# Optimization experiments

Hardware: AMD Instinct MI355X
Metric: run time of the kernel (lower is better)

Reference implementation:

```python
import jax, jax.numpy as jnp
import numpy as np

D_MODEL = 1024
D_INNER = 2048   # expand=2
D_STATE = 16
D_CONV = 4
DT_RANK = 64     # ceil(d_model/16)
BATCH = 4
SEQLEN = 2048


def setup_inputs() -> dict:
    key = jax.random.key(0)
    ks = jax.random.split(key, 9)
    f = lambda k, shape, s=0.02: jax.random.normal(k, shape, dtype=jnp.float32) * s
    return {
        "x": jax.random.normal(ks[0], (BATCH, SEQLEN, D_MODEL), dtype=jnp.float32),
        "norm_w": jnp.ones((D_MODEL,), jnp.float32),
        "in_proj_w": f(ks[1], (2 * D_INNER, D_MODEL)),
        "conv_w": f(ks[2], (D_INNER, D_CONV), 0.1),
        "conv_b": f(ks[3], (D_INNER,), 0.1),
        "x_proj_w": f(ks[4], (DT_RANK + 2 * D_STATE, D_INNER)),
        "dt_proj_w": f(ks[5], (D_INNER, DT_RANK), 0.1),
        "dt_proj_b": f(ks[6], (D_INNER,), 0.1),
        "A_log": jnp.log(jnp.tile(jnp.arange(1, D_STATE + 1, dtype=jnp.float32), (D_INNER, 1))),
        "D_param": jnp.ones((D_INNER,), jnp.float32),
        "out_proj_w": f(ks[7], (D_MODEL, D_INNER)),
    }


def _rmsnorm(x, w):
    eps = jnp.finfo(jnp.float32).eps
    var = jnp.mean(x * x, axis=-1, keepdims=True)
    return x * jax.lax.rsqrt(var + eps) * w


def _mamba(x_norm, in_proj_w, conv_w, conv_b, x_proj_w,
           dt_proj_w, dt_proj_b, A_log, D_param, out_proj_w):
    B, L, _ = x_norm.shape
    # input projection -> [B, L, 2*D_INNER], split into x and gate z
    xz = jnp.einsum('bld,ed->ble', x_norm, in_proj_w)
    x_in, z = jnp.split(xz, 2, axis=-1)
    # causal depthwise conv1d (kernel D_CONV, left pad D_CONV-1)
    x_c = jax.lax.conv_general_dilated(
        x_in.transpose(0, 2, 1),                 # [B, D_INNER, L]
        conv_w[:, None, :],                      # [D_INNER, 1, D_CONV]
        window_strides=(1,), padding=[(D_CONV - 1, 0)],
        dimension_numbers=('NCH', 'OIH', 'NCH'),
        feature_group_count=D_INNER,
    ) + conv_b[None, :, None]
    u = jax.nn.silu(x_c.transpose(0, 2, 1))      # [B, L, D_INNER]
    # SSM parameters
    x_dbl = jnp.einsum('bld,ed->ble', u, x_proj_w)  # [B, L, DT_RANK+2*D_STATE]
    dt, B_mat, C_mat = jnp.split(x_dbl, [DT_RANK, DT_RANK + D_STATE], axis=-1)
    dt = jax.nn.softplus(jnp.einsum('blr,dr->bld', dt, dt_proj_w) + dt_proj_b)  # [B,L,D_INNER]
    A = -jnp.exp(A_log)                          # [D_INNER, D_STATE]

    # selective scan over time; state h: [B, D_INNER, D_STATE]
    def step(h, inputs):
        dt_t, B_t, C_t, u_t = inputs             # [B,Dn],[B,S],[B,S],[B,Dn]
        dA = jnp.exp(dt_t[:, :, None] * A)       # [B, Dn, S]
        h = dA * h + (dt_t * u_t)[:, :, None] * B_t[:, None, :]
        y_t = jnp.einsum('bds,bs->bd', h, C_t)
        return h, y_t

    h0 = jnp.zeros((B, D_INNER, D_STATE), x_norm.dtype)
    xs = (dt.transpose(1, 0, 2), B_mat.transpose(1, 0, 2),
          C_mat.transpose(1, 0, 2), u.transpose(1, 0, 2))
    _, ys = jax.lax.scan(step, h0, xs)           # [L, B, D_INNER]
    y = ys.transpose(1, 0, 2) + D_param * u
    y = y * jax.nn.silu(z)
    return jnp.einsum('bld,ed->ble', y, out_proj_w)  # [B, L, D_MODEL]


def reference(x, norm_w, in_proj_w, conv_w, conv_b, x_proj_w,
              dt_proj_w, dt_proj_b, A_log, D_param, out_proj_w):
    x_norm = _rmsnorm(x, norm_w)
    out = _mamba(x_norm, in_proj_w, conv_w, conv_b, x_proj_w,
                 dt_proj_w, dt_proj_b, A_log, D_param, out_proj_w)
    return x + out
```

## Files before the change

kernel.cpp:

```cpp
#include <hip/hip_runtime.h>
#include <hip/hip_bf16.h>
#include <math.h>

#define DM 1024
#define DI 2048
#define DS 16
#define DC 4
#define DR 64
#define NB 4
#define SL 2048
#define BL (NB * SL)
#define DXP (DR + 2 * DS)
#define NC 32
#define CL (SL / NC)
#define XNS 8

typedef __hip_bfloat16 bf16;
typedef __attribute__((ext_vector_type(8))) short short8;
typedef __attribute__((ext_vector_type(4))) float floatx4;
typedef unsigned int u32;

__device__ __forceinline__ float to_f(float v) { return v; }
__device__ __forceinline__ float to_f(bf16 v) { return __bfloat162float(v); }
template <typename T> __device__ __forceinline__ T from_f(float v);
template <> __device__ __forceinline__ float from_f<float>(float v) { return v; }
template <> __device__ __forceinline__ bf16 from_f<bf16>(float v) { return __float2bfloat16(v); }

__device__ __forceinline__ float bfbits2f(unsigned short u) {
  u32 b = ((u32)u) << 16;
  return __builtin_bit_cast(float, b);
}
__device__ __forceinline__ ushort f2bfbits(float v) {
  bf16 b = __float2bfloat16(v);
  return (ushort)__builtin_bit_cast(short, b);
}
__device__ __forceinline__ float fsilu(float v) {
  return v * __builtin_amdgcn_rcpf(1.f + __expf(-v));
}

__device__ __forceinline__ void gload16(const ushort* g, ushort* l) {
  __builtin_amdgcn_global_load_lds((const __attribute__((address_space(1))) void*)g,
                                   (__attribute__((address_space(3))) void*)l,
                                   16, 0, 0);
}

__device__ __forceinline__ void vmw6() { asm volatile("s_waitcnt vmcnt(6)" ::: "memory"); }
__device__ __forceinline__ void vmw4() { asm volatile("s_waitcnt vmcnt(4)" ::: "memory"); }
__device__ __forceinline__ void vmw2() { asm volatile("s_waitcnt vmcnt(2)" ::: "memory"); }
__device__ __forceinline__ void vmw0() { asm volatile("s_waitcnt vmcnt(0)" ::: "memory"); }
__device__ __forceinline__ void barx() {
  asm volatile("" ::: "memory");
  __builtin_amdgcn_s_barrier();
  asm volatile("" ::: "memory");
}

__global__ __launch_bounds__(256) void f2b_k(const float* __restrict__ src,
                                             bf16* __restrict__ dst, int n) {
  int i = blockIdx.x * 256 + threadIdx.x;
  if (i < n) dst[i] = from_f<bf16>(src[i]);
}

__global__ __launch_bounds__(256) void rmsnorm_k(const float* __restrict__ x,
                                                 const float* __restrict__ w,
                                                 bf16* __restrict__ o) {
  int row = blockIdx.x;
  const float4* xr = (const float4*)(x + (size_t)row * DM);
  float4 v = xr[threadIdx.x];
  float ss = v.x * v.x + v.y * v.y + v.z * v.z + v.w * v.w;
  for (int off = 32; off > 0; off >>= 1) ss += __shfl_down(ss, off);
  __shared__ float sred[4];
  __shared__ float sscale;
  if ((threadIdx.x & 63) == 0) sred[threadIdx.x >> 6] = ss;
  __syncthreads();
  if (threadIdx.x == 0) {
    float t = sred[0] + sred[1] + sred[2] + sred[3];
    sscale = rsqrtf(t / (float)DM + 1.1920929e-7f);
  }
  __syncthreads();
  float sc = sscale;
  float4 wv = ((const float4*)w)[threadIdx.x];
  ushort4 pk;
  pk.x = f2bfbits(v.x * sc * wv.x);
  pk.y = f2bfbits(v.y * sc * wv.y);
  pk.z = f2bfbits(v.z * sc * wv.z);
  pk.w = f2bfbits(v.w * sc * wv.w);
  ((ushort4*)((ushort*)o + (size_t)row * DM))[threadIdx.x] = pk;
}

template <int MODE>
__global__ __launch_bounds__(512, 1) void gemm256(const bf16* __restrict__ A,
                                                  const bf16* __restrict__ W,
                                                  int M, int N, int K,
                                                  bf16* __restrict__ Cx,
                                                  bf16* __restrict__ Cz, int nsplit,
                                                  float* __restrict__ Cf,
                                                  const float* __restrict__ R) {
  __shared__ ushort SH[65536];
  const int tid = threadIdx.x;
  const int lane = tid & 63, wv = tid >> 6;
  const int wr = wv >> 2, wc = wv & 3;
  const int row15 = lane & 15, quad = lane >> 4;

  int ntm = M >> 8, ntn = N >> 8, nwg = ntm * ntn;
  int bid = blockIdx.x;
  int swz = (bid & 7) * (nwg >> 3) + (bid >> 3);
  int bm0 = (swz / ntn) << 8, bn0 = (swz % ntn) << 8;

  const int nt = K >> 6;
  const ushort* Au = (const ushort*)A;
  const ushort* Wu = (const ushort*)W;

  const int w4u = lane ^ (((lane >> 5) & 1) << 1);
  const int Wsw = (((row15 << 6) | (quad << 4)) ^ (((row15 >> 3) & 1) << 5));
  const char* SHb = (const char*)SH;
  const int Abase0 = (wr << 14) + Wsw;
  const int Abase1 = 32768 + (wr << 14) + Wsw;
  const int Bbase0 = 65536 + ((wc >> 1) << 14) + ((wc & 1) << 13) + Wsw;
  const int Bbase1 = Bbase0 + 32768;

  auto stageA = [&](int tt, int half, int buf) {
    const ushort* g = Au + (size_t)(bm0 + half * 128) * K + tt * 64;
    char* lds = (char*)SH + (size_t)(buf * 2 + half) * 16384;
#pragma unroll
    for (int i = 0; i < 2; ++i) {
      int sub = wv + i * 8;
      int r = ((sub >> 1) << 4) | (w4u >> 2);
      int ce = ((sub & 1) << 5) | ((w4u & 3) << 3);
      gload16(g + (size_t)r * K + ce, (ushort*)(lds + sub * 1024));
    }
  };
  auto stageB = [&](int tt, int half, int buf) {
    const ushort* g = Wu + (size_t)(bn0 + half * 128) * K + tt * 64;
    char* lds = (char*)SH + 65536 + (size_t)(buf * 2 + half) * 16384;
#pragma unroll
    for (int i = 0; i < 2; ++i) {
      int sub = wv + i * 8;
      int r = ((sub >> 1) << 4) | (w4u >> 2);
      int ce = ((sub & 1) << 5) | ((w4u & 3) << 3);
      gload16(g + (size_t)r * K + ce, (ushort*)(lds + sub * 1024));
    }
  };

  short8 a_f[4][2], bq[2][2][2];
  floatx4 acc[8][4] = {};

#define LDA_(base, mh) do { _Pragma("unroll") for (int mi = 0; mi < 4; ++mi) \
  { _Pragma("unroll") for (int kk = 0; kk < 2; ++kk) \
    a_f[mi][kk] = *(const short8*)(SHb + (base) + ((((mh)*4 + mi)*2 + kk) << 10)); } } while (0)
#define LDB_(base, nh) do { _Pragma("unroll") for (int ni = 0; ni < 2; ++ni) \
  { _Pragma("unroll") for (int kk = 0; kk < 2; ++kk) \
    bq[nh][ni][kk] = *(const short8*)(SHb + (base) + (((((nh)*2 + ni)*2 + kk)) << 10)); } } while (0)
#define MM_(mh, nh) do { __builtin_amdgcn_s_setprio(1); \
  _Pragma("unroll") for (int mi = 0; mi < 4; ++mi) \
  { _Pragma("unroll") for (int ni = 0; ni < 2; ++ni) \
    { _Pragma("unroll") for (int kk = 0; kk < 2; ++kk) \
      acc[(mh)*4+mi][(nh)*2+ni] = __builtin_amdgcn_mfma_f32_16x16x32_bf16( \
          bq[nh][ni][kk], a_f[mi][kk], acc[(mh)*4+mi][(nh)*2+ni], 0, 0, 0); } } \
  __builtin_amdgcn_s_setprio(0); } while (0)

#define TILE_(t, AB, BB, BBn, curbuf, nxtbuf) do { \
  int tp1 = (t) + 1, tp2 = (t) + 2; \
   \
  LDA_(AB, 0); \
  if (tp1 < nt) stageA(tp1, 0, nxtbuf); \
  barx(); MM_(0, 0); barx(); \
   \
  LDB_(BB, 1); \
  if (tp1 < nt) stageA(tp1, 1, nxtbuf); \
  barx(); MM_(0, 1); barx(); \
   \
  LDA_(AB, 1); \
  if (tp2 < nt) stageB(tp2, 0, curbuf); \
  barx(); MM_(1, 0); \
  if (tp1 < nt) { if (tp2 < nt) vmw6(); else vmw4(); } \
  barx(); \
   \
  if (tp1 < nt) LDB_(BBn, 0); \
  if (tp2 < nt) stageB(tp2, 1, curbuf); \
  barx(); MM_(1, 1); \
  if (tp2 < nt) vmw4(); else vmw0(); \
  barx(); \
} while (0)

  stageB(0, 0, 0); stageB(0, 1, 0); stageA(0, 0, 0); stageA(0, 1, 0);
  stageB(1, 0, 1); stageB(1, 1, 1);
  vmw4();
  barx();
  LDB_(Bbase0, 0);

  for (int t = 0; t < nt; t += 2) {
    TILE_(t,     Abase0, Bbase0, Bbase1, 0, 1);
    TILE_(t + 1, Abase1, Bbase1, Bbase0, 1, 0);
  }
#undef TILE_
#undef MM_
#undef LDB_
#undef LDA_

#pragma unroll
  for (int mi8 = 0; mi8 < 8; ++mi8) {
    int grow = bm0 + wr * 128 + mi8 * 16 + row15;
#pragma unroll
    for (int ni4 = 0; ni4 < 4; ++ni4) {
      int gc = bn0 + wc * 64 + ni4 * 16 + quad * 4;
      floatx4 v = acc[mi8][ni4];
      if (MODE == 1) {
        if (gc < nsplit) {
          ushort4 pk = {f2bfbits(v[0]), f2bfbits(v[1]), f2bfbits(v[2]), f2bfbits(v[3])};
          *(ushort4*)((ushort*)Cx + (size_t)grow * DI + gc) = pk;
        } else {
          ushort4 pk = {f2bfbits(fsilu(v[0])), f2bfbits(fsilu(v[1])),
                        f2bfbits(fsilu(v[2])), f2bfbits(fsilu(v[3]))};
          *(ushort4*)((ushort*)Cz + (size_t)grow * DI + (gc - nsplit)) = pk;
        }
      } else {
        size_t o = (size_t)grow * N + gc;
        float4 r4 = *(const float4*)&R[o];
        float4 o4 = {v[0] + r4.x, v[1] + r4.y, v[2] + r4.z, v[3] + r4.w};
        *(float4*)&Cf[o] = o4;
      }
    }
  }
}

template <int MODE>
__global__ __launch_bounds__(512, 1) void gemm_np(const bf16* __restrict__ A,
                                                  const bf16* __restrict__ W,
                                                  int M, int N, int K,
                                                  bf16* __restrict__ Cx,
                                                  bf16* __restrict__ Cz, int nsplit,
                                                  float* __restrict__ Cf,
                                                  const float* __restrict__ R) {
  __shared__ ushort SH[49152];
  const int tid = threadIdx.x;
  const int lane = tid & 63, wv = tid >> 6;
  const int wr = wv >> 1, wc = wv & 1;
  const int row15 = lane & 15, quad = lane >> 4;

  int ntm = M >> 8, ntn = N >> 7, nwg = ntm * ntn;
  int bid = blockIdx.x;
  int swz = (bid & 7) * (nwg >> 3) + (bid >> 3);
  int bm0 = (swz / ntn) << 8, bn0 = (swz % ntn) << 7;

  const int nt = K >> 6;
  const ushort* Au = (const ushort*)A;
  const ushort* Wu = (const ushort*)W;
  const ushort* Ag = Au + (u32)bm0 * (u32)K;
  const ushort* Bg = Wu + (u32)bn0 * (u32)K;

  const int w4u = lane ^ (((lane >> 5) & 1) << 1);
  const int sub0 = wv, sub1 = wv + 8;
  const int r0 = ((sub0 >> 1) << 4) | (w4u >> 2);
  const int c0 = ((sub0 & 1) << 5) | ((w4u & 3) << 3);
  const int r1 = ((sub1 >> 1) << 4) | (w4u >> 2);
  const int c1 = ((sub1 & 1) << 5) | ((w4u & 3) << 3);
  ushort* shA = (ushort*)SH;
  ushort* shB = (ushort*)SH + 32768;

  auto stage = [&](const ushort* gbase, int rowoff, int tt, ushort* lbase) {
    gload16(gbase + (u32)(rowoff + r0) * (u32)K + (u32)(tt * 64 + c0), lbase + (sub0 << 9));
    gload16(gbase + (u32)(rowoff + r1) * (u32)K + (u32)(tt * 64 + c1), lbase + (sub1 << 9));
  };

  const int Wsw = (((row15 << 6) | (quad << 4)) ^ (((row15 >> 3) & 1) << 5));
  const char* SHb = (const char*)SH;
  const int AB0 = (wr << 13) + Wsw;
  const int AB1 = 32768 + AB0;
  const int BB0 = 65536 + (wc << 13) + Wsw;
  const int BB1 = BB0 + 16384;

  short8 a0[2][2], a1[2][2], bq0A[2][2], bq0B[2][2], bq1[2][2];
  floatx4 acc[4][4] = {};

#define LDA_(dst, base, mh) do { _Pragma("unroll") for (int i_ = 0; i_ < 2; ++i_) \
  { _Pragma("unroll") for (int kk = 0; kk < 2; ++kk) \
    dst[i_][kk] = *(const short8*)(SHb + (base) + ((((mh)*2 + i_)*2 + kk) << 10)); } } while (0)
#define LDB_(dst, base, nh) do { _Pragma("unroll") for (int j_ = 0; j_ < 2; ++j_) \
  { _Pragma("unroll") for (int kk = 0; kk < 2; ++kk) \
    dst[j_][kk] = *(const short8*)(SHb + (base) + ((((nh)*2 + j_)*2 + kk) << 10)); } } while (0)
#define MM_(aset, bset, mh, nh) do { __builtin_amdgcn_s_setprio(1); \
  _Pragma("unroll") for (int i_ = 0; i_ < 2; ++i_) \
  { _Pragma("unroll") for (int j_ = 0; j_ < 2; ++j_) \
    { _Pragma("unroll") for (int kk = 0; kk < 2; ++kk) \
      acc[(mh)*2+i_][(nh)*2+j_] = __builtin_amdgcn_mfma_f32_16x16x32_bf16( \
          bset[j_][kk], aset[i_][kk], acc[(mh)*2+i_][(nh)*2+j_], 0, 0, 0); } } \
  __builtin_amdgcn_s_setprio(0); } while (0)

#define TILE_(t, ABc, BBc, ABn, BBn, BQU, BQF, CURB, NXTB) do { \
  int tp1 = (t) + 1, tp2 = (t) + 2; \
   \
  LDB_(bq1, BBc, 1); \
  if (tp1 < nt) stage(Ag, 0, tp1, shA + (NXTB) * 16384); \
  barx(); MM_(a0, BQU, 0, 0); barx(); \
   \
  LDA_(a1, ABc, 1); \
  if (tp1 < nt) stage(Ag, 128, tp1, shA + (NXTB) * 16384 + 8192); \
  barx(); MM_(a0, bq1, 0, 1); barx(); \
   \
  if (tp2 < nt) stage(Bg, 0, tp2, shB + (CURB) * 8192); \
  barx(); MM_(a1, bq1, 1, 1); \
  if (tp2 < nt) vmw2(); else vmw0(); \
  barx(); \
   \
  if (tp1 < nt) { LDA_(a0, ABn, 0); LDB_(BQF, BBn, 0); } \
  barx(); MM_(a1, BQU, 1, 0); barx(); \
} while (0)

  stage(Bg, 0, 0, shB);
  stage(Ag, 0, 0, shA);
  stage(Ag, 128, 0, shA + 8192);
  if (nt > 1) { stage(Bg, 0, 1, shB + 8192); vmw2(); } else { vmw0(); }
  barx();
  LDA_(a0, AB0, 0);
  LDB_(bq0A, BB0, 0);

  for (int t = 0; t < nt; t += 2) {
    TILE_(t,     AB0, BB0, AB1, BB1, bq0A, bq0B, 0, 1);
    TILE_(t + 1, AB1, BB1, AB0, BB0, bq0B, bq0A, 1, 0);
  }
#undef TILE_
#undef MM_
#undef LDB_
#undef LDA_

#pragma unroll
  for (int mi = 0; mi < 4; ++mi) {
    int grow = bm0 + wr * 64 + mi * 16 + row15;
#pragma unroll
    for (int ni = 0; ni < 4; ++ni) {
      int gc = bn0 + wc * 64 + ni * 16 + quad * 4;
      floatx4 v = acc[mi][ni];
      if (MODE == 1) {
        if (gc < nsplit) {
          ushort4 pk = {f2bfbits(v[0]), f2bfbits(v[1]), f2bfbits(v[2]), f2bfbits(v[3])};
          *(ushort4*)((ushort*)Cx + (size_t)grow * DI + gc) = pk;
        } else {
          ushort4 pk = {f2bfbits(fsilu(v[0])), f2bfbits(fsilu(v[1])),
                        f2bfbits(fsilu(v[2])), f2bfbits(fsilu(v[3]))};
          *(ushort4*)((ushort*)Cz + (size_t)grow * DI + (gc - nsplit)) = pk;
        }
      } else {
        size_t o = (size_t)grow * N + gc;
        float4 r4 = *(const float4*)&R[o];
        float4 o4 = {v[0] + r4.x, v[1] + r4.y, v[2] + r4.z, v[3] + r4.w};
        *(float4*)&Cf[o] = o4;
      }
    }
  }
}

#define TM 128
#define TN 128
#define TK 32
#define LDK 40
template <int MODE>
__global__ __launch_bounds__(256) void gemm_mfma(const bf16* __restrict__ A,
                                                 const bf16* __restrict__ W,
                                                 int M, int N, int K,
                                                 bf16* __restrict__ Cx,
                                                 bf16* __restrict__ Cz, int nsplit,
                                                 float* __restrict__ Cf,
                                                 const float* __restrict__ R,
                                                 const float* __restrict__ bias) {
  __shared__ ushort Asm[TM][TK];
  __shared__ ushort Bsm[TN][TK];
  int bm = blockIdx.y * TM, bn = blockIdx.x * TN;
  int tid = threadIdx.x;
  int lane = tid & 63, wave = tid >> 6;
  int wm = (wave & 1) * 64, wn = (wave >> 1) * 64;
  int row15 = lane & 15, quad = lane >> 4;

  int srow = lane >> 2;
  int scol = (lane & 3) * 8;
  int s0 = wave * 2, s1 = wave * 2 + 1;

  const ushort* Au = (const ushort*)A;
  const ushort* Wu = (const ushort*)W;
  const ushort* ag0 = Au + (size_t)(bm + s0 * 16 + srow) * K + scol;
  const ushort* ag1 = Au + (size_t)(bm + s1 * 16 + srow) * K + scol;
  const ushort* bg0 = Wu + (size_t)(bn + s0 * 16 + srow) * K + scol;
  const ushort* bg1 = Wu + (size_t)(bn + s1 * 16 + srow) * K + scol;
  ushort* la0 = &Asm[s0 * 16][0];
  ushort* la1 = &Asm[s1 * 16][0];
  ushort* lb0 = &Bsm[s0 * 16][0];
  ushort* lb1 = &Bsm[s1 * 16][0];

  floatx4 acc[4][4] = {};

  for (int k0 = 0; k0 < K; k0 += TK) {
    gload16(ag0 + k0, la0);
    gload16(ag1 + k0, la1);
    gload16(bg0 + k0, lb0);
    gload16(bg1 + k0, lb1);
    __syncthreads();
    short8 a_f[4], b_f[4];
#pragma unroll
    for (int i = 0; i < 4; ++i)
      a_f[i] = *(const short8*)&Asm[wm + i * 16 + row15][quad * 8];
#pragma unroll
    for (int j = 0; j < 4; ++j)
      b_f[j] = *(const short8*)&Bsm[wn + j * 16 + row15][quad * 8];
#pragma unroll
    for (int i = 0; i < 4; ++i)
#pragma unroll
      for (int j = 0; j < 4; ++j)
        acc[i][j] = __builtin_amdgcn_mfma_f32_16x16x32_bf16(b_f[j], a_f[i], acc[i][j], 0, 0, 0);
    __syncthreads();
  }
#pragma unroll
  for (int mi = 0; mi < 4; ++mi) {
    int grow = bm + wm + mi * 16 + row15;
#pragma unroll
    for (int ni = 0; ni < 4; ++ni) {
      int gc = bn + wn + ni * 16 + quad * 4;
      floatx4 v = acc[mi][ni];
      if (MODE == 1) {
        if (gc < nsplit) {
          ushort4 pk = {f2bfbits(v[0]), f2bfbits(v[1]), f2bfbits(v[2]), f2bfbits(v[3])};
          *(ushort4*)((ushort*)Cx + (size_t)grow * DI + gc) = pk;
        } else {
          ushort4 pk = {f2bfbits(fsilu(v[0])), f2bfbits(fsilu(v[1])),
                        f2bfbits(fsilu(v[2])), f2bfbits(fsilu(v[3]))};
          *(ushort4*)((ushort*)Cz + (size_t)grow * DI + (gc - nsplit)) = pk;
        }
      } else if (MODE == 2) {
        size_t o = (size_t)grow * N + gc;
        float4 r4 = *(const float4*)&R[o];
        float4 o4 = {v[0] + r4.x, v[1] + r4.y, v[2] + r4.z, v[3] + r4.w};
        *(float4*)&Cf[o] = o4;
      } else {
        float4 b4 = *(const float4*)&bias[gc];
        float t0 = v[0] + b4.x, t1 = v[1] + b4.y, t2 = v[2] + b4.z, t3 = v[3] + b4.w;
        float s0_ = (t0 > 20.f) ? t0 : __logf(1.f + __expf(t0));
        float s1_ = (t1 > 20.f) ? t1 : __logf(1.f + __expf(t1));
        float s2_ = (t2 > 20.f) ? t2 : __logf(1.f + __expf(t2));
        float s3_ = (t3 > 20.f) ? t3 : __logf(1.f + __expf(t3));
        ushort4 pk = {f2bfbits(s0_), f2bfbits(s1_), f2bfbits(s2_), f2bfbits(s3_)};
        *(ushort4*)((ushort*)Cx + (size_t)grow * N + gc) = pk;
      }
    }
  }
}

__global__ __launch_bounds__(256) void xproj_k(const bf16* __restrict__ u,
                                               const bf16* __restrict__ w,
                                               float* __restrict__ Ppart) {
  __shared__ ushort Asm[128][LDK];
  __shared__ ushort Bsm[96][LDK];
  int kbase = blockIdx.x * (DI / XNS);
  int bm = blockIdx.y * 128;
  int tid = threadIdx.x;
  int lane = tid & 63, wave = tid >> 6;
  int row15 = lane & 15, quad = lane >> 4;
  int srow = tid >> 1, skoff = (tid & 1) * 16;

  floatx4 acc[2][6] = {};
  const ushort* Au = (const ushort*)u;
  const ushort* Wu = (const ushort*)w;
  for (int k0 = kbase; k0 < kbase + (DI / XNS); k0 += TK) {
    const ushort* ag = Au + (size_t)(bm + srow) * DI + k0 + skoff;
    *(short8*)&Asm[srow][skoff]     = *(const short8*)ag;
    *(short8*)&Asm[srow][skoff + 8] = *(const short8*)(ag + 8);
    if (tid < 192) {
      const ushort* wg = Wu + (size_t)srow * DI + k0 + skoff;
      *(short8*)&Bsm[srow][skoff]     = *(const short8*)wg;
      *(short8*)&Bsm[srow][skoff + 8] = *(const short8*)(wg + 8);
    }
    __syncthreads();
    short8 a_f[2], b_f[6];
#pragma unroll
    for (int i = 0; i < 2; ++i)
      a_f[i] = *(const short8*)&Asm[wave * 32 + i * 16 + row15][quad * 8];
#pragma unroll
    for (int j = 0; j < 6; ++j)
      b_f[j] = *(const short8*)&Bsm[j * 16 + row15][quad * 8];
#pragma unroll
    for (int i = 0; i < 2; ++i)
#pragma unroll
      for (int j = 0; j < 6; ++j)
        acc[i][j] = __builtin_amdgcn_mfma_f32_16x16x32_bf16(b_f[j], a_f[i], acc[i][j], 0, 0, 0);
    __syncthreads();
  }
  float* P = Ppart + (size_t)blockIdx.x * ((size_t)BL * DXP);
#pragma unroll
  for (int mi = 0; mi < 2; ++mi) {
    int grow = bm + wave * 32 + mi * 16 + row15;
#pragma unroll
    for (int nj = 0; nj < 6; ++nj) {
      int gc = nj * 16 + quad * 4;
      floatx4 v = acc[mi][nj];
      float4 o4 = {v[0], v[1], v[2], v[3]};
      *(float4*)&P[(size_t)grow * DXP + gc] = o4;
    }
  }
}

__global__ __launch_bounds__(256) void xred_k(const float* __restrict__ Ppart,
                                              float* __restrict__ xdbl,
                                              bf16* __restrict__ dtin) {
  int i = blockIdx.x * 256 + threadIdx.x;
  float s = 0.f;
#pragma unroll
  for (int p = 0; p < XNS; ++p) s += Ppart[(size_t)p * ((size_t)BL * DXP) + i];
  xdbl[i] = s;
  int r = i / DXP, c = i - r * DXP;
  if (c < DR) dtin[r * DR + c] = from_f<bf16>(s);
}

#define TSTRIP 8
__global__ __launch_bounds__(256) void conv_silu_k(const bf16* __restrict__ xin,
                                                   const float* __restrict__ cw,
                                                   const float* __restrict__ cb,
                                                   bf16* __restrict__ u) {
  int blk = blockIdx.x;
  int b = blk >> 8;
  int l0 = (blk & 255) * TSTRIP;
  int c0 = threadIdx.x * 8;

  float4 cw4[8];
  const float4* cwp = (const float4*)cw;
#pragma unroll
  for (int j = 0; j < 8; ++j) cw4[j] = cwp[c0 + j];
  float cbv[8];
  {
    float4 cb0 = *(const float4*)&cb[c0];
    float4 cb1 = *(const float4*)&cb[c0 + 4];
    cbv[0] = cb0.x; cbv[1] = cb0.y; cbv[2] = cb0.z; cbv[3] = cb0.w;
    cbv[4] = cb1.x; cbv[5] = cb1.y; cbv[6] = cb1.z; cbv[7] = cb1.w;
  }

  const ushort* base = (const ushort*)xin + ((size_t)(b * SL + l0) * DI + c0);
  ushort* ubase = (ushort*)u + ((size_t)(b * SL + l0) * DI + c0);

  short8 zz = {};
  short8 w0 = zz, w1 = zz, w2 = zz;
  if (l0 >= 3) {
    w0 = *(const short8*)(base - 3 * DI);
    w1 = *(const short8*)(base - 2 * DI);
    w2 = *(const short8*)(base - 1 * DI);
  }
#pragma unroll
  for (int l = 0; l < TSTRIP; ++l) {
    short8 w3 = *(const short8*)(base + (ptrdiff_t)l * DI);
    short8 outv;
#pragma unroll
    for (int j = 0; j < 8; ++j) {
      float a = cbv[j]
              + bfbits2f((unsigned short)w0[j]) * cw4[j].x
              + bfbits2f((unsigned short)w1[j]) * cw4[j].y
              + bfbits2f((unsigned short)w2[j]) * cw4[j].z
              + bfbits2f((unsigned short)w3[j]) * cw4[j].w;
      outv[j] = (short)f2bfbits(fsilu(a));
    }
    *(short8*)(ubase + (ptrdiff_t)l * DI) = outv;
    w0 = w1; w1 = w2; w2 = w3;
  }
}

__global__ __launch_bounds__(256) void scan_p1(const bf16* __restrict__ dts,
                                               const bf16* __restrict__ u,
                                               const float* __restrict__ xdbl,
                                               const float* __restrict__ A_log,
                                               float* __restrict__ Pbuf,
                                               float* __restrict__ Qbuf) {
  int bid = blockIdx.x;
  int b = bid >> 8;
  int c = (bid >> 3) & (NC - 1);
  int d = (bid & 7) * 256 + threadIdx.x;

  float A[DS], h[DS], P[DS];
#pragma unroll
  for (int s = 0; s < DS; ++s) {
    A[s] = -__expf(A_log[d * DS + s]);
    h[s] = 0.f; P[s] = 1.f;
  }
  size_t bl0 = (size_t)b * SL + c * CL;
  size_t base = bl0 * DI + d;
  size_t xb = bl0 * DXP + DR;
  for (int l = 0; l < CL; ++l) {
    float dtv = to_f(dts[base]);
    float uv = to_f(u[base]);
    float du = dtv * uv;
    float Bv[16];
    *(float4*)&Bv[0]  = *(const float4*)(xdbl + xb);
    *(float4*)&Bv[4]  = *(const float4*)(xdbl + xb + 4);
    *(float4*)&Bv[8]  = *(const float4*)(xdbl + xb + 8);
    *(float4*)&Bv[12] = *(const float4*)(xdbl + xb + 12);
#pragma unroll
    for (int s = 0; s < DS; ++s) {
      float dA = __expf(dtv * A[s]);
      h[s] = dA * h[s] + du * Bv[s];
      P[s] *= dA;
    }
    base += DI;
    xb += DXP;
  }
  size_t o = ((size_t)(b * NC + c) * DS) * DI + d;
#pragma unroll
  for (int s = 0; s < DS; ++s) {
    Pbuf[o + (size_t)s * DI] = P[s];
    Qbuf[o + (size_t)s * DI] = h[s];
  }
}

__global__ __launch_bounds__(256) void scan_p2(float* __restrict__ Pbuf,
                                               float* __restrict__ Qbuf) {
  int bid = blockIdx.x;
  int b = bid >> 7;
  int s = (bid >> 3) & (DS - 1);
  int d = (bid & 7) * 256 + threadIdx.x;
  float h = 0.f;
  for (int c = 0; c < NC; ++c) {
    size_t idx = ((size_t)((b * NC + c) * DS + s)) * DI + d;
    float Pv = Pbuf[idx];
    float qv = Qbuf[idx];
    Qbuf[idx] = h;
    h = Pv * h + qv;
  }
}

__global__ __launch_bounds__(256) void scan_p3(const bf16* __restrict__ dts,
                                               bf16* __restrict__ u,
                                               const float* __restrict__ xdbl,
                                               const float* __restrict__ A_log,
                                               const float* __restrict__ Dp,
                                               const bf16* __restrict__ g,
                                               const float* __restrict__ Qbuf) {
  int bid = blockIdx.x;
  int b = bid >> 8;
  int c = (bid >> 3) & (NC - 1);
  int d = (bid & 7) * 256 + threadIdx.x;

  float A[DS], h[DS];
  size_t o = ((size_t)(b * NC + c) * DS) * DI + d;
#pragma unroll
  for (int s = 0; s < DS; ++s) {
    A[s] = -__expf(A_log[d * DS + s]);
    h[s] = Qbuf[o + (size_t)s * DI];
  }
  float Dd = Dp[d];
  size_t bl0 = (size_t)b * SL + c * CL;
  size_t base = bl0 * DI + d;
  size_t xb = bl0 * DXP + DR;
  for (int l = 0; l < CL; ++l) {
    float dtv = to_f(dts[base]);
    float uv = to_f(u[base]);
    float gv = to_f(g[base]);
    float du = dtv * uv;
    float Bv[16], Cv[16];
    *(float4*)&Bv[0]  = *(const float4*)(xdbl + xb);
    *(float4*)&Bv[4]  = *(const float4*)(xdbl + xb + 4);
    *(float4*)&Bv[8]  = *(const float4*)(xdbl + xb + 8);
    *(float4*)&Bv[12] = *(const float4*)(xdbl + xb + 12);
    *(float4*)&Cv[0]  = *(const float4*)(xdbl + xb + DS);
    *(float4*)&Cv[4]  = *(const float4*)(xdbl + xb + DS + 4);
    *(float4*)&Cv[8]  = *(const float4*)(xdbl + xb + DS + 8);
    *(float4*)&Cv[12] = *(const float4*)(xdbl + xb + DS + 12);
    float p0 = 0.f, p1 = 0.f, p2 = 0.f, p3 = 0.f;
#pragma unroll
    for (int s = 0; s < DS; s += 4) {
      float dA0 = __expf(dtv * A[s + 0]);
      float dA1 = __expf(dtv * A[s + 1]);
      float dA2 = __expf(dtv * A[s + 2]);
      float dA3 = __expf(dtv * A[s + 3]);
      h[s + 0] = dA0 * h[s + 0] + du * Bv[s + 0];
      h[s + 1] = dA1 * h[s + 1] + du * Bv[s + 1];
      h[s + 2] = dA2 * h[s + 2] + du * Bv[s + 2];
      h[s + 3] = dA3 * h[s + 3] + du * Bv[s + 3];
      p0 += h[s + 0] * Cv[s + 0];
      p1 += h[s + 1] * Cv[s + 1];
      p2 += h[s + 2] * Cv[s + 2];
      p3 += h[s + 3] * Cv[s + 3];
    }
    float yv = ((p0 + p1) + (p2 + p3)) + Dd * uv;
    u[base] = from_f<bf16>(yv * gv);
    base += DI;
    xb += DXP;
  }
}

extern "C" void kernel_launch(void* const* d_in, const int* in_sizes, int n_in,
                              void* d_out, int out_size, void* d_ws, size_t ws_size,
                              hipStream_t stream) {
  const float* x        = (const float*)d_in[0];
  const float* norm_w   = (const float*)d_in[1];
  const float* in_projw = (const float*)d_in[2];
  const float* conv_w   = (const float*)d_in[3];
  const float* conv_b   = (const float*)d_in[4];
  const float* x_projw  = (const float*)d_in[5];
  const float* dt_projw = (const float*)d_in[6];
  const float* dt_projb = (const float*)d_in[7];
  const float* A_log    = (const float*)d_in[8];
  const float* Dp       = (const float*)d_in[9];
  const float* out_projw= (const float*)d_in[10];
  float* out = (float*)d_out;

  char* wsb = (char*)d_ws;
  bf16* x_buf  = (bf16*)wsb;
  bf16* z_buf  = (bf16*)(wsb + (size_t)BL * DI * 2);
  bf16* u_buf  = (bf16*)(wsb + (size_t)BL * DI * 4);
  char* ovl    = wsb + (size_t)BL * DI * 6;
  bf16* ipw_bf = (bf16*)ovl;
  float* xdbl   = (float*)ovl;
  bf16*  xpw_bf = (bf16*)(ovl + 3145728);
  bf16*  dtw_bf = (bf16*)(ovl + 3538944);
  bf16*  dtin_bf= (bf16*)(ovl + 3801088);
  bf16* xnorm_bf = u_buf;
  bf16* dt_buf   = x_buf;
  bf16* opw_bf   = x_buf;
  float* Ppart = out;
  float* Pbuf = out;
  float* Qbuf = out + (size_t)NB * NC * DS * DI;

  f2b_k<<<(2 * DI * DM) / 256, 256, 0, stream>>>(in_projw, ipw_bf, 2 * DI * DM);
  rmsnorm_k<<<BL, 256, 0, stream>>>(x, norm_w, xnorm_bf);
  gemm256<1><<<(BL / 256) * (2 * DI / 256), 512, 0, stream>>>(
      xnorm_bf, ipw_bf, BL, 2 * DI, DM, x_buf, z_buf, DI, nullptr, nullptr);
  conv_silu_k<<<NB * (SL / TSTRIP), 256, 0, stream>>>(x_buf, conv_w, conv_b, u_buf);
  f2b_k<<<(DXP * DI + 255) / 256, 256, 0, stream>>>(x_projw, xpw_bf, DXP * DI);
  f2b_k<<<(DI * DR) / 256, 256, 0, stream>>>(dt_projw, dtw_bf, DI * DR);
  xproj_k<<<dim3(XNS, BL / 128), 256, 0, stream>>>(u_buf, xpw_bf, Ppart);
  xred_k<<<(BL * DXP) / 256, 256, 0, stream>>>(Ppart, xdbl, dtin_bf);
  gemm_mfma<3><<<dim3(DI / TN, BL / TM), 256, 0, stream>>>(
      dtin_bf, dtw_bf, BL, DI, DR, dt_buf, nullptr, 0, nullptr, nullptr, dt_projb);
  scan_p1<<<NB * NC * (DI / 256), 256, 0, stream>>>(dt_buf, u_buf, xdbl, A_log, Pbuf, Qbuf);
  scan_p2<<<NB * DS * (DI / 256), 256, 0, stream>>>(Pbuf, Qbuf);
  scan_p3<<<NB * NC * (DI / 256), 256, 0, stream>>>(dt_buf, u_buf, xdbl, A_log, Dp, z_buf, Qbuf);
  f2b_k<<<(DM * DI) / 256, 256, 0, stream>>>(out_projw, opw_bf, DM * DI);
  gemm_np<2><<<(BL / 256) * (DM / 128), 512, 0, stream>>>(
      u_buf, opw_bf, BL, DM, DI, nullptr, nullptr, 0, out, x);
}
```

Measured before the change: 431.6 us.

## Prefetch A tiles two steps ahead in both bf16 GEMM pipelines

Both MFMA GEMM kernels change their global-to-LDS prefetch schedule so that A tiles are staged two iterations ahead into the current buffer, as B tiles already were. This deepens the pipeline: more loads are in flight and the vmcnt waits are relaxed accordingly. It also drops the early B-fragment register preload for the next tile in the large kernel. The aim is to hide more global-load latency behind MFMA work. In exchange, the LDS buffer reuse becomes more delicate, and more outstanding loads may add issue pressure.

```diff
diff --git a/kernel.cpp b/kernel.cpp
--- a/kernel.cpp
+++ b/kernel.cpp
@@ -46,7 +46,6 @@
 
 __device__ __forceinline__ void vmw6() { asm volatile("s_waitcnt vmcnt(6)" ::: "memory"); }
 __device__ __forceinline__ void vmw4() { asm volatile("s_waitcnt vmcnt(4)" ::: "memory"); }
-__device__ __forceinline__ void vmw2() { asm volatile("s_waitcnt vmcnt(2)" ::: "memory"); }
 __device__ __forceinline__ void vmw0() { asm volatile("s_waitcnt vmcnt(0)" ::: "memory"); }
 __device__ __forceinline__ void barx() {
   asm volatile("" ::: "memory");
@@ -158,39 +157,34 @@
           bq[nh][ni][kk], a_f[mi][kk], acc[(mh)*4+mi][(nh)*2+ni], 0, 0, 0); } } \
   __builtin_amdgcn_s_setprio(0); } while (0)
 
-#define TILE_(t, AB, BB, BBn, curbuf, nxtbuf) do { \
+#define TILE_(t, AB, BB, curbuf, nxtbuf) do { \
   int tp1 = (t) + 1, tp2 = (t) + 2; \
    \
-  LDA_(AB, 0); \
-  if (tp1 < nt) stageA(tp1, 0, nxtbuf); \
+  LDA_(AB, 0); LDB_(BB, 0); \
+  if (tp1 < nt) stageA(tp1, 1, nxtbuf); \
   barx(); MM_(0, 0); barx(); \
    \
   LDB_(BB, 1); \
-  if (tp1 < nt) stageA(tp1, 1, nxtbuf); \
   barx(); MM_(0, 1); barx(); \
    \
   LDA_(AB, 1); \
   if (tp2 < nt) stageB(tp2, 0, curbuf); \
-  barx(); MM_(1, 0); \
-  if (tp1 < nt) { if (tp2 < nt) vmw6(); else vmw4(); } \
-  barx(); \
+  barx(); MM_(1, 0); barx(); \
    \
-  if (tp1 < nt) LDB_(BBn, 0); \
-  if (tp2 < nt) stageB(tp2, 1, curbuf); \
+  if (tp2 < nt) { stageA(tp2, 0, curbuf); stageB(tp2, 1, curbuf); } \
   barx(); MM_(1, 1); \
-  if (tp2 < nt) vmw4(); else vmw0(); \
+  if (tp2 < nt) vmw6(); else vmw0(); \
   barx(); \
 } while (0)
 
   stageB(0, 0, 0); stageB(0, 1, 0); stageA(0, 0, 0); stageA(0, 1, 0);
-  stageB(1, 0, 1); stageB(1, 1, 1);
-  vmw4();
+  if (nt > 1) { stageB(1, 0, 1); stageB(1, 1, 1); stageA(1, 0, 1); vmw6(); }
+  else vmw0();
   barx();
-  LDB_(Bbase0, 0);
 
   for (int t = 0; t < nt; t += 2) {
-    TILE_(t,     Abase0, Bbase0, Bbase1, 0, 1);
-    TILE_(t + 1, Abase1, Bbase1, Bbase0, 1, 0);
+    TILE_(t, Abase0, Bbase0, 0, 1);
+    TILE_(t + 1, Abase1, Bbase1, 1, 0);
   }
 #undef TILE_
 #undef MM_
@@ -286,37 +280,42 @@
           bset[j_][kk], aset[i_][kk], acc[(mh)*2+i_][(nh)*2+j_], 0, 0, 0); } } \
   __builtin_amdgcn_s_setprio(0); } while (0)
 
-#define TILE_(t, ABc, BBc, ABn, BBn, BQU, BQF, CURB, NXTB) do { \
+#define TILE_(t, ABc, BBc, ABn, BBn, BQU, BQF, CURB) do { \
   int tp1 = (t) + 1, tp2 = (t) + 2; \
    \
   LDB_(bq1, BBc, 1); \
-  if (tp1 < nt) stage(Ag, 0, tp1, shA + (NXTB) * 16384); \
   barx(); MM_(a0, BQU, 0, 0); barx(); \
    \
   LDA_(a1, ABc, 1); \
-  if (tp1 < nt) stage(Ag, 128, tp1, shA + (NXTB) * 16384 + 8192); \
+  if (tp2 < nt) stage(Bg, 0, tp2, shB + (CURB) * 8192); \
   barx(); MM_(a0, bq1, 0, 1); barx(); \
    \
-  if (tp2 < nt) stage(Bg, 0, tp2, shB + (CURB) * 8192); \
+  if (tp2 < nt) stage(Ag, 0, tp2, shA + (CURB) * 16384); \
   barx(); MM_(a1, bq1, 1, 1); \
-  if (tp2 < nt) vmw2(); else vmw0(); \
+  if (tp2 < nt) vmw4(); else vmw0(); \
   barx(); \
    \
   if (tp1 < nt) { LDA_(a0, ABn, 0); LDB_(BQF, BBn, 0); } \
+  if (tp2 < nt) stage(Ag, 128, tp2, shA + (CURB) * 16384 + 8192); \
   barx(); MM_(a1, BQU, 1, 0); barx(); \
 } while (0)
 
   stage(Bg, 0, 0, shB);
   stage(Ag, 0, 0, shA);
   stage(Ag, 128, 0, shA + 8192);
-  if (nt > 1) { stage(Bg, 0, 1, shB + 8192); vmw2(); } else { vmw0(); }
+  if (nt > 1) {
+    stage(Bg, 0, 1, shB + 8192);
+    stage(Ag, 0, 1, shA + 16384);
+    stage(Ag, 128, 1, shA + 16384 + 8192);
+    vmw4();
+  } else vmw0();
   barx();
   LDA_(a0, AB0, 0);
   LDB_(bq0A, BB0, 0);
 
   for (int t = 0; t < nt; t += 2) {
-    TILE_(t,     AB0, BB0, AB1, BB1, bq0A, bq0B, 0, 1);
-    TILE_(t + 1, AB1, BB1, AB0, BB0, bq0B, bq0A, 1, 0);
+    TILE_(t,     AB0, BB0, AB1, BB1, bq0A, bq0B, 0);
+    TILE_(t + 1, AB1, BB1, AB0, BB0, bq0B, bq0A, 1);
   }
 #undef TILE_
 #undef MM_
```

Result: no change. 437.5 us (+1.4%).
